# Kernel tuning notes

Hardware: AMD Instinct MI355X
Metric: run time of the kernel (lower is better)

## Reference

```python
import jax, jax.numpy as jnp
import numpy as np

B, L, N, D = 256, 32, 256 * 32, 768
NEG_INF = -1e30  # stand-in for float('-inf') that is safe under masking
SUPCON_W, REPULSION_W, BCE_W = 1.0, 0.1, 1.0
REPULSION_THRESHOLD = 0.3


def setup_inputs() -> dict:
    key = jax.random.key(0)
    k1, k2, k3 = jax.random.split(key, 3)
    logits = jax.random.normal(k1, (N, 1), dtype=jnp.float32)
    labels = jax.random.randint(k2, (B, L), 0, 2, dtype=jnp.int32)  # 0/1 targets
    batch_indices = jnp.arange(N, dtype=jnp.int64) // L   # each sample has L labels
    label_ids = jnp.arange(N, dtype=jnp.int64) % L + 1    # 1..L per sample
    label_embeddings = jax.random.normal(k3, (N, D), dtype=jnp.float32)
    logit_scale = jnp.full((1,), 2.0, dtype=jnp.float32)
    bce_scale = jnp.ones((1,), dtype=jnp.float32)
    return {
        "logits": logits, "labels": labels, "batch_indices": batch_indices,
        "label_ids": label_ids, "label_embeddings": label_embeddings,
        "logit_scale": logit_scale, "bce_scale": bce_scale,
    }


def _supcon_loss(dense_logits, targets):
    # targets: (B, L) float, -100 marks padding
    mask_valid = targets != -100.0
    targets_clean = jnp.where(mask_valid, targets, 0.0)
    pos_mask = (targets_clean > 0.5).astype(dense_logits.dtype)
    num_pos = pos_mask.sum(axis=1)                      # (B,)
    has_pos = num_pos > 0
    logits_masked = jnp.where(mask_valid, dense_logits, NEG_INF)
    log_probs = jax.nn.log_softmax(logits_masked, axis=1)
    sum_log_prob_pos = jnp.sum(jnp.where(pos_mask > 0, log_probs, 0.0), axis=1)
    loss_per_sample = -sum_log_prob_pos / (num_pos + 1e-9)
    n_anchor = jnp.maximum(has_pos.sum(), 1)
    return jnp.sum(jnp.where(has_pos, loss_per_sample, 0.0)) / n_anchor


def _label_repulsion_loss(embeddings, label_ids, batch_indices):
    norms = jnp.linalg.norm(embeddings, axis=-1, keepdims=True)
    emb_n = embeddings / jnp.maximum(norms, 1e-12)
    sim = emb_n @ emb_n.T                               # (N, N)
    mask = (label_ids[None, :] != label_ids[:, None]) & (
        batch_indices[None, :] == batch_indices[:, None])
    penalties = jax.nn.relu(sim - REPULSION_THRESHOLD)
    n_valid = jnp.maximum(mask.sum(), 1)
    return jnp.sum(jnp.where(mask, penalties, 0.0)) / n_valid


def _bce_loss(dense_logits, targets, logit_scale, bce_scale):
    mask = targets != -100.0
    raw = dense_logits / (jnp.exp(logit_scale[0]) + 1e-9)
    x = raw * jnp.maximum(jnp.abs(bce_scale[0]), 0.1)
    # stable BCE-with-logits: max(x,0) - x*t + log(1+exp(-|x|))
    per = jnp.maximum(x, 0.0) - x * targets + jnp.log1p(jnp.exp(-jnp.abs(x)))
    n_valid = jnp.maximum(mask.sum(), 1)
    return jnp.sum(jnp.where(mask, per, 0.0)) / n_valid


def reference(logits, labels, batch_indices, label_ids, label_embeddings,
              logit_scale, bce_scale):
    batch_size = labels.shape[0]
    max_label_id = L  # int(label_ids.max()); static here: label_ids span 1..L
    dense_logits = jnp.full((batch_size, max_label_id), NEG_INF, dtype=logits.dtype)
    dense_logits = dense_logits.at[batch_indices, label_ids - 1].set(logits[:, 0])
    targets = labels[:, :max_label_id].astype(jnp.float32)  # valid_cols == L
    total = jnp.float32(0.0)
    total = total + SUPCON_W * _supcon_loss(dense_logits, targets)
    total = total + REPULSION_W * _label_repulsion_loss(
        label_embeddings, label_ids, batch_indices)
    total = total + BCE_W * _bce_loss(dense_logits, targets, logit_scale, bce_scale)
    return total
```

## Files before the change

### kernel.cpp

```cpp
#include <hip/hip_runtime.h>
#include <hip/hip_bf16.h>
#include <math.h>

#define REP_N_VALID 253952.0f
#define BCE_N_VALID 8192.0f

#define KC 256
#define PITCH 260

__global__ __launch_bounds__(256) void rep_kernel(const float* __restrict__ emb,
                                                  float* __restrict__ rep_out) {
    __shared__ float tile[32 * PITCH];
    __shared__ float gram[32 * 32];
    __shared__ float inv_norm[32];
    __shared__ float wsum[4];

    const int t    = threadIdx.x;
    const int g    = blockIdx.x;
    const int kq   = t >> 6;
    const int lane = t & 63;
    const int ty   = lane >> 3;
    const int tx   = lane & 7;

    for (int i = t; i < 1024; i += 256) gram[i] = 0.0f;

    float acc[4][4];
#pragma unroll
    for (int i = 0; i < 4; ++i)
#pragma unroll
        for (int j = 0; j < 4; ++j) acc[i][j] = 0.0f;

    const float* base = emb + (size_t)g * 32 * 768;

    for (int c = 0; c < 3; ++c) {
#pragma unroll
        for (int i = 0; i < 8; ++i) {
            int idx = t + i * 256;
            int row = idx >> 6;
            int c4  = idx & 63;
            float4 v = *(const float4*)(base + row * 768 + c * KC + c4 * 4);
            *(float4*)(&tile[row * PITCH + c4 * 4]) = v;
        }
        __syncthreads();

        const int k0 = kq * 64;
#pragma unroll 4
        for (int s = 0; s < 16; ++s) {
            const int k = k0 + s * 4;
            float4 a[4], b[4];
#pragma unroll
            for (int r = 0; r < 4; ++r)
                a[r] = *(const float4*)(&tile[(ty + 8 * r) * PITCH + k]);
#pragma unroll
            for (int r = 0; r < 4; ++r)
                b[r] = *(const float4*)(&tile[(tx + 8 * r) * PITCH + k]);
#pragma unroll
            for (int i = 0; i < 4; ++i)
#pragma unroll
                for (int j = 0; j < 4; ++j) {
                    acc[i][j] = fmaf(a[i].x, b[j].x, acc[i][j]);
                    acc[i][j] = fmaf(a[i].y, b[j].y, acc[i][j]);
                    acc[i][j] = fmaf(a[i].z, b[j].z, acc[i][j]);
                    acc[i][j] = fmaf(a[i].w, b[j].w, acc[i][j]);
                }
        }
        __syncthreads();
    }

    for (int q = 0; q < 4; ++q) {
        if (kq == q) {
#pragma unroll
            for (int i = 0; i < 4; ++i)
#pragma unroll
                for (int j = 0; j < 4; ++j)
                    gram[(ty + 8 * i) * 32 + (tx + 8 * j)] += acc[i][j];
        }
        __syncthreads();
    }

    if (t < 32) {
        float n = sqrtf(gram[t * 32 + t]);
        inv_norm[t] = 1.0f / fmaxf(n, 1e-12f);
    }
    __syncthreads();

    float psum = 0.0f;
    for (int e = t; e < 1024; e += 256) {
        int i = e >> 5, j = e & 31;
        if (i != j) {
            float sim = gram[e] * inv_norm[i] * inv_norm[j];
            psum += fmaxf(sim - 0.3f, 0.0f);
        }
    }
#pragma unroll
    for (int off = 32; off > 0; off >>= 1) psum += __shfl_down(psum, off, 64);
    if (lane == 0) wsum[kq] = psum;
    __syncthreads();
    if (t == 0) atomicAdd(rep_out, wsum[0] + wsum[1] + wsum[2] + wsum[3]);
}

__global__ __launch_bounds__(256) void finalize_kernel(
        const float* __restrict__ logits, const int* __restrict__ labels,
        const float* __restrict__ logit_scale, const float* __restrict__ bce_scale,
        const float* __restrict__ rep_sum, float* __restrict__ out) {
    __shared__ float lx[8192];
    __shared__ float r0[4], r1[4], r2[4];
    const int t = threadIdx.x;

#pragma unroll
    for (int i = 0; i < 8; ++i) {
        int idx = t + i * 256;
        *(float4*)(&lx[idx * 4]) = *(const float4*)(&logits[idx * 4]);
    }
    __syncthreads();

    const float* x   = &lx[t * 32];
    const int*   lab = &labels[t * 32];

    float m = -INFINITY;
    for (int l = 0; l < 32; ++l) m = fmaxf(m, x[l]);
    float se = 0.0f;
    for (int l = 0; l < 32; ++l) se += expf(x[l] - m);
    const float lse = logf(se) + m;

    const float inv_es = 1.0f / (expf(logit_scale[0]) + 1e-9f);
    const float bsc    = fmaxf(fabsf(bce_scale[0]), 0.1f);

    float npos = 0.0f, slp = 0.0f, bce = 0.0f;
    for (int l = 0; l < 32; ++l) {
        float tv = (float)lab[l];
        if (tv > 0.5f) { npos += 1.0f; slp += x[l] - lse; }
        float xx = x[l] * inv_es * bsc;
        bce += fmaxf(xx, 0.0f) - xx * tv + log1pf(expf(-fabsf(xx)));
    }
    float sup = (npos > 0.0f) ? (-slp / (npos + 1e-9f)) : 0.0f;
    float anc = (npos > 0.0f) ? 1.0f : 0.0f;

    float v0 = sup, v1 = anc, v2 = bce;
#pragma unroll
    for (int off = 32; off > 0; off >>= 1) {
        v0 += __shfl_down(v0, off, 64);
        v1 += __shfl_down(v1, off, 64);
        v2 += __shfl_down(v2, off, 64);
    }
    const int wave = t >> 6;
    if ((t & 63) == 0) { r0[wave] = v0; r1[wave] = v1; r2[wave] = v2; }
    __syncthreads();

    if (t == 0) {
        float sup_total = r0[0] + r0[1] + r0[2] + r0[3];
        float anc_total = r1[0] + r1[1] + r1[2] + r1[3];
        float bce_total = r2[0] + r2[1] + r2[2] + r2[3];
        float n_anchor = fmaxf(anc_total, 1.0f);
        float total = 1.0f * (sup_total / n_anchor)
                    + 0.1f * (rep_sum[0] / REP_N_VALID)
                    + 1.0f * (bce_total / BCE_N_VALID);
        out[0] = total;
    }
}

extern "C" void kernel_launch(void* const* d_in, const int* in_sizes, int n_in,
                              void* d_out, int out_size, void* d_ws, size_t ws_size,
                              hipStream_t stream) {
    const float* logits      = (const float*)d_in[0];
    const int*   labels      = (const int*)d_in[1];
    const float* emb         = (const float*)d_in[4];
    const float* logit_scale = (const float*)d_in[5];
    const float* bce_scale   = (const float*)d_in[6];
    float* out     = (float*)d_out;
    float* rep_acc = (float*)d_ws;

    hipMemsetAsync(rep_acc, 0, sizeof(float), stream);
    rep_kernel<<<dim3(256), dim3(256), 0, stream>>>(emb, rep_acc);
    finalize_kernel<<<dim3(1), dim3(256), 0, stream>>>(logits, labels, logit_scale,
                                                       bce_scale, rep_acc, out);
}
```

Before: 114.1 us.

## Replace atomic and memset with per-block partials; pad finalize shared memory

Each rep_kernel block now writes its partial sum to its own workspace slot instead of atomically adding into one accumulator. The finalize kernel reduces those 256 partials, which removes the hipMemsetAsync launch and the atomic contention. The finalize kernel also stages logits and labels into padded shared memory (pitch 33) so the per-thread row reads avoid bank conflicts, and the inner gram loop unroll changes from 4 to 1. The lower unroll may reduce instruction-level parallelism in the FMA loop.

```diff
diff --git a/kernel.cpp b/kernel.cpp
--- a/kernel.cpp
+++ b/kernel.cpp
@@ -9,7 +9,7 @@
 #define PITCH 260
 
 __global__ __launch_bounds__(256) void rep_kernel(const float* __restrict__ emb,
-                                                  float* __restrict__ rep_out) {
+                                                  float* __restrict__ rep_partial) {
     __shared__ float tile[32 * PITCH];
     __shared__ float gram[32 * 32];
     __shared__ float inv_norm[32];
@@ -44,7 +44,7 @@
         __syncthreads();
 
         const int k0 = kq * 64;
-#pragma unroll 4
+#pragma unroll 1
         for (int s = 0; s < 16; ++s) {
             const int k = k0 + s * 4;
             float4 a[4], b[4];
@@ -96,26 +96,40 @@
     for (int off = 32; off > 0; off >>= 1) psum += __shfl_down(psum, off, 64);
     if (lane == 0) wsum[kq] = psum;
     __syncthreads();
-    if (t == 0) atomicAdd(rep_out, wsum[0] + wsum[1] + wsum[2] + wsum[3]);
+    if (t == 0) rep_partial[g] = wsum[0] + wsum[1] + wsum[2] + wsum[3];
 }
+
+#define FP 33
 
 __global__ __launch_bounds__(256) void finalize_kernel(
         const float* __restrict__ logits, const int* __restrict__ labels,
         const float* __restrict__ logit_scale, const float* __restrict__ bce_scale,
-        const float* __restrict__ rep_sum, float* __restrict__ out) {
-    __shared__ float lx[8192];
-    __shared__ float r0[4], r1[4], r2[4];
+        const float* __restrict__ rep_partial, float* __restrict__ out) {
+    __shared__ float lx[256 * FP];
+    __shared__ float lt[256 * FP];
+    __shared__ float r0[4], r1[4], r2[4], r3[4];
     const int t = threadIdx.x;
 
 #pragma unroll
     for (int i = 0; i < 8; ++i) {
         int idx = t + i * 256;
-        *(float4*)(&lx[idx * 4]) = *(const float4*)(&logits[idx * 4]);
+        int row = idx >> 3;
+        int c0  = (idx & 7) * 4;
+        float4 v = *(const float4*)(&logits[idx * 4]);
+        lx[row * FP + c0 + 0] = v.x;
+        lx[row * FP + c0 + 1] = v.y;
+        lx[row * FP + c0 + 2] = v.z;
+        lx[row * FP + c0 + 3] = v.w;
+        int4 lv = *(const int4*)(&labels[idx * 4]);
+        lt[row * FP + c0 + 0] = (float)lv.x;
+        lt[row * FP + c0 + 1] = (float)lv.y;
+        lt[row * FP + c0 + 2] = (float)lv.z;
+        lt[row * FP + c0 + 3] = (float)lv.w;
     }
     __syncthreads();
 
-    const float* x   = &lx[t * 32];
-    const int*   lab = &labels[t * 32];
+    const float* x  = &lx[t * FP];
+    const float* tv = &lt[t * FP];
 
     float m = -INFINITY;
     for (int l = 0; l < 32; ++l) m = fmaxf(m, x[l]);
@@ -128,34 +142,36 @@
 
     float npos = 0.0f, slp = 0.0f, bce = 0.0f;
     for (int l = 0; l < 32; ++l) {
-        float tv = (float)lab[l];
-        if (tv > 0.5f) { npos += 1.0f; slp += x[l] - lse; }
+        float tg = tv[l];
+        if (tg > 0.5f) { npos += 1.0f; slp += x[l] - lse; }
         float xx = x[l] * inv_es * bsc;
-        bce += fmaxf(xx, 0.0f) - xx * tv + log1pf(expf(-fabsf(xx)));
+        bce += fmaxf(xx, 0.0f) - xx * tg + log1pf(expf(-fabsf(xx)));
     }
     float sup = (npos > 0.0f) ? (-slp / (npos + 1e-9f)) : 0.0f;
     float anc = (npos > 0.0f) ? 1.0f : 0.0f;
+    float rep = rep_partial[t];
 
-    float v0 = sup, v1 = anc, v2 = bce;
+    float v0 = sup, v1 = anc, v2 = bce, v3 = rep;
 #pragma unroll
     for (int off = 32; off > 0; off >>= 1) {
         v0 += __shfl_down(v0, off, 64);
         v1 += __shfl_down(v1, off, 64);
         v2 += __shfl_down(v2, off, 64);
+        v3 += __shfl_down(v3, off, 64);
     }
     const int wave = t >> 6;
-    if ((t & 63) == 0) { r0[wave] = v0; r1[wave] = v1; r2[wave] = v2; }
+    if ((t & 63) == 0) { r0[wave] = v0; r1[wave] = v1; r2[wave] = v2; r3[wave] = v3; }
     __syncthreads();
 
     if (t == 0) {
         float sup_total = r0[0] + r0[1] + r0[2] + r0[3];
         float anc_total = r1[0] + r1[1] + r1[2] + r1[3];
         float bce_total = r2[0] + r2[1] + r2[2] + r2[3];
+        float rep_total = r3[0] + r3[1] + r3[2] + r3[3];
         float n_anchor = fmaxf(anc_total, 1.0f);
-        float total = 1.0f * (sup_total / n_anchor)
-                    + 0.1f * (rep_sum[0] / REP_N_VALID)
-                    + 1.0f * (bce_total / BCE_N_VALID);
-        out[0] = total;
+        out[0] = 1.0f * (sup_total / n_anchor)
+               + 0.1f * (rep_total / REP_N_VALID)
+               + 1.0f * (bce_total / BCE_N_VALID);
     }
 }
 
@@ -167,11 +183,10 @@
     const float* emb         = (const float*)d_in[4];
     const float* logit_scale = (const float*)d_in[5];
     const float* bce_scale   = (const float*)d_in[6];
-    float* out     = (float*)d_out;
-    float* rep_acc = (float*)d_ws;
+    float* out         = (float*)d_out;
+    float* rep_partial = (float*)d_ws;
 
-    hipMemsetAsync(rep_acc, 0, sizeof(float), stream);
-    rep_kernel<<<dim3(256), dim3(256), 0, stream>>>(emb, rep_acc);
+    rep_kernel<<<dim3(256), dim3(256), 0, stream>>>(emb, rep_partial);
     finalize_kernel<<<dim3(1), dim3(256), 0, stream>>>(logits, labels, logit_scale,
-                                                       bce_scale, rep_acc, out);
+                                                       bce_scale, rep_partial, out);
 }
```

Result: faster. 105.5 us (-7.5%).

## Fuse per-row supcon/BCE into repulsion kernel and reduce per-block partials

Applied to the files above, without the earlier changes.

Moves the per-sample log-softmax, supcon and BCE terms into the Gram-matrix kernel, one row per block, computed with wave shuffles. Each block writes a float4 partial instead of using a global atomic, so the memset goes away and a tiny reduce kernel sums the 256 partials. The block grows to 512 threads with an 8-way K split, and the serialized Gram accumulation is replaced by LDS atomics. This removes the serial single-block finalize work and a memset launch, at the cost of more LDS atomic contention and fewer unrolled FMAs per thread.

```diff
diff --git a/kernel.cpp b/kernel.cpp
--- a/kernel.cpp
+++ b/kernel.cpp
@@ -8,21 +8,31 @@
 #define KC 256
 #define PITCH 260
 
-__global__ __launch_bounds__(256) void rep_kernel(const float* __restrict__ emb,
-                                                  float* __restrict__ rep_out) {
+__global__ __launch_bounds__(512) void fused_kernel(
+        const float* __restrict__ emb,
+        const float* __restrict__ logits, const int* __restrict__ labels,
+        const float* __restrict__ logit_scale, const float* __restrict__ bce_scale,
+        float4* __restrict__ partials) {
     __shared__ float tile[32 * PITCH];
     __shared__ float gram[32 * 32];
     __shared__ float inv_norm[32];
-    __shared__ float wsum[4];
+    __shared__ float wsum[8];
+    __shared__ float rowres[3];
 
     const int t    = threadIdx.x;
     const int g    = blockIdx.x;
-    const int kq   = t >> 6;
+    const int w    = t >> 6;
     const int lane = t & 63;
     const int ty   = lane >> 3;
     const int tx   = lane & 7;
 
-    for (int i = t; i < 1024; i += 256) gram[i] = 0.0f;
+    float xval = 0.0f; float tgv = 0.0f;
+    if (w == 0 && lane < 32) {
+        xval = logits[g * 32 + lane];
+        tgv  = (float)labels[g * 32 + lane];
+    }
+
+    for (int i = t; i < 1024; i += 512) gram[i] = 0.0f;
 
     float acc[4][4];
 #pragma unroll
@@ -34,8 +44,8 @@
 
     for (int c = 0; c < 3; ++c) {
 #pragma unroll
-        for (int i = 0; i < 8; ++i) {
-            int idx = t + i * 256;
+        for (int i = 0; i < 4; ++i) {
+            int idx = t + i * 512;
             int row = idx >> 6;
             int c4  = idx & 63;
             float4 v = *(const float4*)(base + row * 768 + c * KC + c4 * 4);
@@ -43,9 +53,9 @@
         }
         __syncthreads();
 
-        const int k0 = kq * 64;
-#pragma unroll 4
-        for (int s = 0; s < 16; ++s) {
+        const int k0 = w * 32;
+#pragma unroll 1
+        for (int s = 0; s < 8; ++s) {
             const int k = k0 + s * 4;
             float4 a[4], b[4];
 #pragma unroll
@@ -67,25 +77,54 @@
         __syncthreads();
     }
 
-    for (int q = 0; q < 4; ++q) {
-        if (kq == q) {
 #pragma unroll
-            for (int i = 0; i < 4; ++i)
+    for (int i = 0; i < 4; ++i)
 #pragma unroll
-                for (int j = 0; j < 4; ++j)
-                    gram[(ty + 8 * i) * 32 + (tx + 8 * j)] += acc[i][j];
-        }
-        __syncthreads();
-    }
+        for (int j = 0; j < 4; ++j)
+            atomicAdd(&gram[(ty + 8 * i) * 32 + (tx + 8 * j)], acc[i][j]);
+    __syncthreads();
 
     if (t < 32) {
         float n = sqrtf(gram[t * 32 + t]);
         inv_norm[t] = 1.0f / fmaxf(n, 1e-12f);
     }
+
+    if (w == 0 && lane < 32) {
+        float m = xval;
+#pragma unroll
+        for (int off = 16; off > 0; off >>= 1) m = fmaxf(m, __shfl_xor(m, off, 32));
+        float e = expf(xval - m);
+        float se = e;
+#pragma unroll
+        for (int off = 16; off > 0; off >>= 1) se += __shfl_xor(se, off, 32);
+        const float lse = logf(se) + m;
+
+        const float inv_es = 1.0f / (expf(logit_scale[0]) + 1e-9f);
+        const float bsc    = fmaxf(fabsf(bce_scale[0]), 0.1f);
+
+        float pos  = (tgv > 0.5f) ? 1.0f : 0.0f;
+        float slp  = pos * (xval - lse);
+        float xx   = xval * inv_es * bsc;
+        float bce  = fmaxf(xx, 0.0f) - xx * tgv + log1pf(expf(-fabsf(xx)));
+        float npos = pos;
+#pragma unroll
+        for (int off = 16; off > 0; off >>= 1) {
+            npos += __shfl_xor(npos, off, 32);
+            slp  += __shfl_xor(slp,  off, 32);
+            bce  += __shfl_xor(bce,  off, 32);
+        }
+        if (lane == 0) {
+            rowres[0] = (npos > 0.0f) ? (-slp / (npos + 1e-9f)) : 0.0f;
+            rowres[1] = (npos > 0.0f) ? 1.0f : 0.0f;
+            rowres[2] = bce;
+        }
+    }
     __syncthreads();
 
     float psum = 0.0f;
-    for (int e = t; e < 1024; e += 256) {
+#pragma unroll
+    for (int rr = 0; rr < 2; ++rr) {
+        int e = t + rr * 512;
         int i = e >> 5, j = e & 31;
         if (i != j) {
             float sim = gram[e] * inv_norm[i] * inv_norm[j];
@@ -94,68 +133,40 @@
     }
 #pragma unroll
     for (int off = 32; off > 0; off >>= 1) psum += __shfl_down(psum, off, 64);
-    if (lane == 0) wsum[kq] = psum;
+    if (lane == 0) wsum[w] = psum;
     __syncthreads();
-    if (t == 0) atomicAdd(rep_out, wsum[0] + wsum[1] + wsum[2] + wsum[3]);
+
+    if (t == 0) {
+        float rep = wsum[0] + wsum[1] + wsum[2] + wsum[3]
+                  + wsum[4] + wsum[5] + wsum[6] + wsum[7];
+        partials[g] = make_float4(rep, rowres[0], rowres[1], rowres[2]);
+    }
 }
 
-__global__ __launch_bounds__(256) void finalize_kernel(
-        const float* __restrict__ logits, const int* __restrict__ labels,
-        const float* __restrict__ logit_scale, const float* __restrict__ bce_scale,
-        const float* __restrict__ rep_sum, float* __restrict__ out) {
-    __shared__ float lx[8192];
-    __shared__ float r0[4], r1[4], r2[4];
+__global__ __launch_bounds__(256) void reduce_kernel(
+        const float4* __restrict__ partials, float* __restrict__ out) {
+    __shared__ float r0[4], r1[4], r2[4], r3[4];
     const int t = threadIdx.x;
-
-#pragma unroll
-    for (int i = 0; i < 8; ++i) {
-        int idx = t + i * 256;
-        *(float4*)(&lx[idx * 4]) = *(const float4*)(&logits[idx * 4]);
-    }
-    __syncthreads();
-
-    const float* x   = &lx[t * 32];
-    const int*   lab = &labels[t * 32];
-
-    float m = -INFINITY;
-    for (int l = 0; l < 32; ++l) m = fmaxf(m, x[l]);
-    float se = 0.0f;
-    for (int l = 0; l < 32; ++l) se += expf(x[l] - m);
-    const float lse = logf(se) + m;
-
-    const float inv_es = 1.0f / (expf(logit_scale[0]) + 1e-9f);
-    const float bsc    = fmaxf(fabsf(bce_scale[0]), 0.1f);
-
-    float npos = 0.0f, slp = 0.0f, bce = 0.0f;
-    for (int l = 0; l < 32; ++l) {
-        float tv = (float)lab[l];
-        if (tv > 0.5f) { npos += 1.0f; slp += x[l] - lse; }
-        float xx = x[l] * inv_es * bsc;
-        bce += fmaxf(xx, 0.0f) - xx * tv + log1pf(expf(-fabsf(xx)));
-    }
-    float sup = (npos > 0.0f) ? (-slp / (npos + 1e-9f)) : 0.0f;
-    float anc = (npos > 0.0f) ? 1.0f : 0.0f;
-
-    float v0 = sup, v1 = anc, v2 = bce;
+    float4 p = partials[t];
+    float v0 = p.x, v1 = p.y, v2 = p.z, v3 = p.w;
 #pragma unroll
     for (int off = 32; off > 0; off >>= 1) {
         v0 += __shfl_down(v0, off, 64);
         v1 += __shfl_down(v1, off, 64);
         v2 += __shfl_down(v2, off, 64);
+        v3 += __shfl_down(v3, off, 64);
     }
     const int wave = t >> 6;
-    if ((t & 63) == 0) { r0[wave] = v0; r1[wave] = v1; r2[wave] = v2; }
+    if ((t & 63) == 0) { r0[wave] = v0; r1[wave] = v1; r2[wave] = v2; r3[wave] = v3; }
     __syncthreads();
-
     if (t == 0) {
-        float sup_total = r0[0] + r0[1] + r0[2] + r0[3];
-        float anc_total = r1[0] + r1[1] + r1[2] + r1[3];
-        float bce_total = r2[0] + r2[1] + r2[2] + r2[3];
-        float n_anchor = fmaxf(anc_total, 1.0f);
-        float total = 1.0f * (sup_total / n_anchor)
-                    + 0.1f * (rep_sum[0] / REP_N_VALID)
-                    + 1.0f * (bce_total / BCE_N_VALID);
-        out[0] = total;
+        float rep = r0[0] + r0[1] + r0[2] + r0[3];
+        float sup = r1[0] + r1[1] + r1[2] + r1[3];
+        float anc = r2[0] + r2[1] + r2[2] + r2[3];
+        float bce = r3[0] + r3[1] + r3[2] + r3[3];
+        out[0] = sup / fmaxf(anc, 1.0f)
+               + 0.1f * (rep / REP_N_VALID)
+               + bce / BCE_N_VALID;
     }
 }
 
@@ -167,11 +178,10 @@
     const float* emb         = (const float*)d_in[4];
     const float* logit_scale = (const float*)d_in[5];
     const float* bce_scale   = (const float*)d_in[6];
-    float* out     = (float*)d_out;
-    float* rep_acc = (float*)d_ws;
+    float*  out      = (float*)d_out;
+    float4* partials = (float4*)d_ws;
 
-    hipMemsetAsync(rep_acc, 0, sizeof(float), stream);
-    rep_kernel<<<dim3(256), dim3(256), 0, stream>>>(emb, rep_acc);
-    finalize_kernel<<<dim3(1), dim3(256), 0, stream>>>(logits, labels, logit_scale,
-                                                       bce_scale, rep_acc, out);
+    fused_kernel<<<dim3(256), dim3(512), 0, stream>>>(emb, logits, labels,
+                                                      logit_scale, bce_scale, partials);
+    reduce_kernel<<<dim3(1), dim3(256), 0, stream>>>(partials, out);
 }
```

Result: faster. 100.3 us (-12.1%).
